# Optimization experiments

Measured on AMD Instinct MI355X. Metric: run time of the kernel, lower is better.

The kernel has to match this reference:

```python
import jax, jax.numpy as jnp
import numpy as np
from jax.scipy.special import gammaln, xlogy

B, L, C = 8, 1024, 1536
H, KD, VD = 8, 64, 192
NF = 192              # num_features for relative positional basis
FS = NF // 6          # feat_size per basis family (each family emits 2*FS cols)
SCALE = KD ** -0.5


def _pos_basis(seq_len):
    """Enformer-style basis: [exp, central_mask, gamma], each concat'd with sign copy.
    Returns [2*seq_len-1, NF] float32 constants (no learnable params)."""
    positions = jnp.arange(-(seq_len - 1), seq_len, dtype=jnp.float32)
    seq_length = float(seq_len)
    ap = jnp.abs(positions)[:, None]                      # [2L-1, 1]
    # exponential decay features
    half_life = 2.0 ** jnp.linspace(3.0, np.log2(seq_length), FS)
    f_exp = jnp.exp(-jnp.log(2.0) / half_life * ap)       # [2L-1, FS]
    # central mask features
    cw = 2.0 ** jnp.arange(1, FS + 1, dtype=jnp.float32) - 1.0
    f_cm = (cw > ap).astype(jnp.float32)
    # gamma pdf features
    stddev = seq_length / (2.0 * FS)
    start_mean = seq_length / FS
    mean = jnp.linspace(start_mean, seq_length, FS)
    conc = (mean / stddev) ** 2
    rate = mean / stddev ** 2
    log_pdf = xlogy(conc - 1.0, ap) - rate * ap - gammaln(conc) + conc * jnp.log(rate)
    pdf = jnp.exp(log_pdf) + 1e-8
    f_g = pdf / jnp.max(pdf)
    sign = jnp.sign(positions)[:, None]
    feats = [f_exp, f_cm, f_g]
    return jnp.concatenate([jnp.concatenate([f, sign * f], axis=-1) for f in feats], axis=-1)


def _rel_shift(x):
    # x: [b, h, s, f]; Transformer-XL relative shift via pad+reshape.
    b, h, s, f = x.shape
    x = jnp.pad(x, ((0, 0), (0, 0), (0, 0), (1, 0)))
    x = x.reshape(b, h, f + 1, s)
    return x[:, :, 1:s + 1, :]


def setup_inputs() -> dict:
    key = jax.random.key(0)
    ks = jax.random.split(key, 12)
    s_in = C ** -0.5
    s_hv = (H * VD) ** -0.5
    s_nf = NF ** -0.5
    return {
        "x":  jax.random.normal(ks[0], (B, L, C), jnp.float32),
        "Wq": jax.random.normal(ks[1], (C, H * KD), jnp.float32) * s_in,
        "bq": jnp.zeros((H * KD,), jnp.float32),
        "Wk": jax.random.normal(ks[2], (C, H * KD), jnp.float32) * s_in,
        "bk": jnp.zeros((H * KD,), jnp.float32),
        "Wv": jax.random.normal(ks[3], (C, H * VD), jnp.float32) * s_in,
        "bv": jnp.zeros((H * VD,), jnp.float32),
        "Wo": jax.random.normal(ks[4], (H * VD, C), jnp.float32) * s_hv,
        "bo": jnp.zeros((C,), jnp.float32),
        "WR": jax.random.normal(ks[5], (NF, KD), jnp.float32) * s_nf,
        "u":  jax.random.normal(ks[6], (H, KD), jnp.float32) * 0.02,
        "v":  jax.random.normal(ks[7], (H, KD), jnp.float32) * 0.02,
    }


def reference(x, Wq, bq, Wk, bk, Wv, bv, Wo, bo, WR, u, v):
    b, s, c = x.shape
    Q = (x @ Wq + bq).reshape(b, s, H, KD).transpose(0, 2, 1, 3)   # [b,h,s,kd]
    K = (x @ Wk + bk).reshape(b, s, H, KD).transpose(0, 2, 1, 3)
    V = (x @ Wv + bv).reshape(b, s, H, VD).transpose(0, 2, 1, 3)
    R = _pos_basis(s) @ WR                                          # [2s-1, kd]
    term1 = jnp.einsum('bhqd,bhkd->bhqk', Q, K)                     # content-content
    term2 = _rel_shift(jnp.einsum('bhqd,rd->bhqr', Q, R))           # content-position
    term3 = jnp.einsum('hd,bhkd->bhk', u, K)[:, :, None, :]         # global content bias
    term4 = _rel_shift(jnp.einsum('hd,rd->hr', v, R)[None, :, None, :])  # [1,h,1,1]
    attn = jax.nn.softmax((term1 + term2 + term3 + term4) * SCALE, axis=-1)
    out = jnp.einsum('bhqk,bhkv->bhqv', attn, V)
    out = out.transpose(0, 2, 1, 3).reshape(b, s, H * VD)
    return out @ Wo + bo
```

## Files before the change

### kernel.cpp

```cpp
#include <hip/hip_runtime.h>
#include <cstdint>
#include <cstddef>

typedef float f32x4 __attribute__((ext_vector_type(4)));
typedef short bf16x8 __attribute__((ext_vector_type(8)));

#define DEVI __device__ __forceinline__

namespace {

constexpr int BB = 8, LL = 1024, CC = 1536;
constexpr int HH = 8, KDIM = 64, VDIM = 192;
constexpr int NFEAT = 192, FSZ = 32;
constexpr float SCL = 0.125f;
constexpr int MR = BB * LL;
constexpr int NQK = HH * KDIM;
constexpr int NVD = HH * VDIM;
constexpr int NQKV = 2 * NQK + NVD;

DEVI short f2bf(float f) {
  unsigned u = __float_as_uint(f);
  u = (u + 0x7FFFu + ((u >> 16) & 1u)) >> 16;
  return (short)u;
}

DEVI void gload_lds16(const void* g, void* l) {
  __builtin_amdgcn_global_load_lds(
      (const __attribute__((address_space(1))) void*)g,
      (__attribute__((address_space(3))) void*)l, 16, 0, 0);
}

__global__ void k_f32_to_bf16(const float* __restrict__ src, short* __restrict__ dst, int n) {
  int i0 = (blockIdx.x * blockDim.x + threadIdx.x) * 4;
  int stride = gridDim.x * blockDim.x * 4;
  for (int i = i0; i < n; i += stride) {
    float4 v = *reinterpret_cast<const float4*>(src + i);
    short4 o = { f2bf(v.x), f2bf(v.y), f2bf(v.z), f2bf(v.w) };
    *reinterpret_cast<short4*>(dst + i) = o;
  }
}

__global__ void k_transpose_all(const float* __restrict__ s0, short* __restrict__ d0,
                                const float* __restrict__ s1, short* __restrict__ d1,
                                const float* __restrict__ s2, short* __restrict__ d2,
                                const float* __restrict__ s3, short* __restrict__ d3) {
  __shared__ float tile[32][33];
  int idx = blockIdx.x;
  const float* src; short* dst; int R, Cd, gx, local;
  if (idx < 768)       { src = s0; dst = d0; R = CC;  Cd = NQK; gx = 16; local = idx; }
  else if (idx < 1536) { src = s1; dst = d1; R = CC;  Cd = NQK; gx = 16; local = idx - 768; }
  else if (idx < 3840) { src = s2; dst = d2; R = CC;  Cd = NVD; gx = 48; local = idx - 1536; }
  else                 { src = s3; dst = d3; R = NVD; Cd = CC;  gx = 48; local = idx - 3840; }
  int c0 = (local % gx) * 32, r0 = (local / gx) * 32;
  int tx = threadIdx.x, ty = threadIdx.y;
  #pragma unroll
  for (int i = 0; i < 4; i++)
    tile[ty + i * 8][tx] = src[(size_t)(r0 + ty + i * 8) * Cd + c0 + tx];
  __syncthreads();
  #pragma unroll
  for (int i = 0; i < 4; i++)
    dst[(size_t)(c0 + ty + i * 8) * R + r0 + tx] = f2bf(tile[tx][ty + i * 8]);
}

__global__ void k_pdfmax(unsigned* slot) {
  int tid = blockIdx.x * blockDim.x + threadIdx.x;
  int nth = gridDim.x * blockDim.x;
  double lmax = 0.0;
  for (int idx = tid; idx < 2047 * FSZ; idx += nth) {
    int j = idx >> 5, i = idx & 31;
    double ap = (double)(j >= 1023 ? j - 1023 : 1023 - j);
    double mean = 32.0 + 32.0 * (double)i;
    double conc = (mean * (1.0 / 16.0)) * (mean * (1.0 / 16.0));
    double rate = mean * (1.0 / 256.0);
    double lp = (conc - 1.0) * log(ap) - rate * ap - lgamma(conc) + conc * log(rate);
    double pdf = exp(lp) + 1e-8;
    lmax = fmax(lmax, pdf);
  }
  float fv = (float)lmax;
  #pragma unroll
  for (int o = 32; o > 0; o >>= 1) fv = fmaxf(fv, __shfl_down(fv, o, 64));
  if ((threadIdx.x & 63) == 0) atomicMax(slot, __float_as_uint(fv));
}

__global__ void k_build_r(const float* __restrict__ WR, const unsigned* __restrict__ slot,
                          short* __restrict__ rbuf) {
  __shared__ float feats[NFEAT];
  int jp = blockIdx.x;
  int tid = threadIdx.x;
  if (jp == 0) {
    if (tid < KDIM) rbuf[tid] = 0;
    return;
  }
  int j = jp - 1;
  int pos = j - (LL - 1);
  int api = pos < 0 ? -pos : pos;
  double ap = (double)api;
  float sgn = pos > 0 ? 1.0f : (pos < 0 ? -1.0f : 0.0f);
  if (tid < FSZ) {
    double xhl = 3.0 + 7.0 * (double)tid / 31.0;
    double hl = exp2(xhl);
    float fe = (float)exp2(-ap / hl);
    feats[tid] = fe; feats[FSZ + tid] = sgn * fe;
  } else if (tid < 2 * FSZ) {
    int i = tid - FSZ;
    double cw = exp2((double)(i + 1)) - 1.0;
    float fc = cw > ap ? 1.0f : 0.0f;
    feats[2 * FSZ + i] = fc; feats[3 * FSZ + i] = sgn * fc;
  } else if (tid < 3 * FSZ) {
    int i = tid - 2 * FSZ;
    double mean = 32.0 + 32.0 * (double)i;
    double conc = (mean * (1.0 / 16.0)) * (mean * (1.0 / 16.0));
    double rate = mean * (1.0 / 256.0);
    double lp = (conc - 1.0) * log(ap) - rate * ap - lgamma(conc) + conc * log(rate);
    double pdf = exp(lp) + 1e-8;
    float fg = (float)(pdf / (double)__uint_as_float(*slot));
    feats[4 * FSZ + i] = fg; feats[5 * FSZ + i] = sgn * fg;
  }
  __syncthreads();
  if (tid < KDIM) {
    float acc = 0.f;
    #pragma unroll 4
    for (int f = 0; f < NFEAT; f++) acc += feats[f] * WR[f * KDIM + tid];
    rbuf[jp * KDIM + tid] = f2bf(acc);
  }
}

template<int MODE>
__global__ __launch_bounds__(256, 2)
void k_gemm2(const short* __restrict__ A, const short* __restrict__ Bt,
             int Ndim, int Kdim,
             const float* __restrict__ c0, const float* __restrict__ c1,
             const float* __restrict__ c2, const float* __restrict__ c3,
             void* __restrict__ D0, void* __restrict__ D1,
             void* __restrict__ D2, void* __restrict__ D3) {
  __shared__ short sA[2][128][64];
  __shared__ short sB[2][128][64];

  int bid = blockIdx.x;
  int xcd = bid & 7;
  int s = bid >> 3;
  int mt = xcd * 8 + (s & 7);
  int nt = s >> 3;
  int m0 = mt * 128, n0 = nt * 128;
  int tid = threadIdx.x;
  int w = tid >> 6, l = tid & 63;
  int hi = l >> 4, lc = l & 15;
  int wr = (w >> 1) * 64, wc = (w & 1) * 64;

  int srow = l >> 3;
  int schunk = ((l & 7) ^ srow) * 8;
  const short* gA = A + (size_t)(m0 + srow) * Kdim + schunk;
  const short* gB = Bt + (size_t)(n0 + srow) * Kdim + schunk;

  f32x4 acc[4][4] = {};
  int T = Kdim >> 6;

  auto stage = [&](int d, int k0) {
    #pragma unroll
    for (int j = 0; j < 4; j++) {
      int rb = (j * 4 + w) * 8;
      gload_lds16(gA + (size_t)rb * Kdim + k0, &sA[d][rb][0]);
      gload_lds16(gB + (size_t)rb * Kdim + k0, &sB[d][rb][0]);
    }
  };

  stage(0, 0);
  __syncthreads();

  int swz8 = (lc & 7) << 3;
  for (int t = 0; t < T; ++t) {
    int buf = t & 1;
    if (t + 1 < T) stage(buf ^ 1, (t + 1) << 6);

    #pragma unroll
    for (int kk = 0; kk < 2; kk++) {
      bf16x8 af[4], bfr[4];
      #pragma unroll
      for (int ni = 0; ni < 4; ni++)
        bfr[ni] = *(const bf16x8*)&sB[buf][wc + ni * 16 + lc][(kk * 32 + hi * 8) ^ swz8];
      #pragma unroll
      for (int mi = 0; mi < 4; mi++)
        af[mi] = *(const bf16x8*)&sA[buf][wr + mi * 16 + lc][(kk * 32 + hi * 8) ^ swz8];
      __builtin_amdgcn_s_setprio(1);
      #pragma unroll
      for (int mi = 0; mi < 4; mi++)
        #pragma unroll
        for (int ni = 0; ni < 4; ni++)
          acc[mi][ni] = __builtin_amdgcn_mfma_f32_16x16x32_bf16(af[mi], bfr[ni], acc[mi][ni], 0, 0, 0);
      __builtin_amdgcn_s_setprio(0);
    }
    __syncthreads();
  }

  #pragma unroll
  for (int ni = 0; ni < 4; ni++) {
    int col = n0 + wc + ni * 16 + lc;
    if (MODE == 0) {
      if (col < NQK) {
        float bb = c0[col], uv = c3[col];
        #pragma unroll
        for (int mi = 0; mi < 4; mi++)
          #pragma unroll
          for (int rr = 0; rr < 4; rr++) {
            int row = m0 + wr + mi * 16 + hi * 4 + rr;
            float v = acc[mi][ni][rr] + bb;
            ((short*)D0)[(size_t)row * NQK + col] = f2bf(v * SCL);
            ((short*)D1)[(size_t)row * NQK + col] = f2bf((v + uv) * SCL);
          }
      } else if (col < 2 * NQK) {
        int c = col - NQK;
        float bb = c1[c];
        #pragma unroll
        for (int mi = 0; mi < 4; mi++)
          #pragma unroll
          for (int rr = 0; rr < 4; rr++) {
            int row = m0 + wr + mi * 16 + hi * 4 + rr;
            ((short*)D2)[(size_t)row * NQK + c] = f2bf(acc[mi][ni][rr] + bb);
          }
      } else {
        int c = col - 2 * NQK;
        int hh = c / VDIM, vv = c - hh * VDIM;
        float bb = c2[c];
        int bI = m0 >> 10;
        short* vt = (short*)D3 + ((size_t)(bI * 8 + hh) * VDIM + vv) * LL;
        int sbase = (m0 & (LL - 1)) + wr + hi * 4;
        #pragma unroll
        for (int mi = 0; mi < 4; mi++) {
          short4 o = { f2bf(acc[mi][ni][0] + bb), f2bf(acc[mi][ni][1] + bb),
                       f2bf(acc[mi][ni][2] + bb), f2bf(acc[mi][ni][3] + bb) };
          *(short4*)&vt[sbase + mi * 16] = o;
        }
      }
    } else {
      float bb = c0[col];
      #pragma unroll
      for (int mi = 0; mi < 4; mi++)
        #pragma unroll
        for (int rr = 0; rr < 4; rr++) {
          int row = m0 + wr + mi * 16 + hi * 4 + rr;
          ((float*)D0)[(size_t)row * Ndim + col] = acc[mi][ni][rr] + bb;
        }
    }
  }
}

__global__ __launch_bounds__(256, 2)
void k_attn(const short* __restrict__ Qp, const short* __restrict__ Qs,
            const short* __restrict__ Kb, const short* __restrict__ Vt,
            const short* __restrict__ Rb, short* __restrict__ AO) {
  __shared__ short sK[2][64][64];
  __shared__ short sV[2][192][64];
  __shared__ short sP[128][64];

  int bid = blockIdx.x;
  int swz = (bid & 7) * 64 + (bid >> 3);
  int qt = swz & 7, bh = swz >> 3;
  int b = bh >> 3, h = bh & 7;
  int q0 = qt * 128;
  int tid = threadIdx.x;
  int w = tid >> 6, l = tid & 63;
  int hi = l >> 4, lc = l & 15;

  int base = (w & 1) * 64;
  int par = w >> 1;
  int rbase = par ? 0 : 1024;

  bf16x8 aq1[2][2], aq2[2][2];
  #pragma unroll
  for (int mi = 0; mi < 2; mi++) {
    int qglob = q0 + base + par + 2 * (mi * 16 + lc);
    const short* qpg = Qp + (size_t)(b * LL + qglob) * NQK + h * KDIM;
    aq1[mi][0] = *(const bf16x8*)&qpg[hi * 8];
    aq1[mi][1] = *(const bf16x8*)&qpg[32 + hi * 8];
    int qsrow = q0 / 2 + base / 2 + par + mi * 16 + lc;
    const short* qsg = Qs + (size_t)(b * LL + qsrow) * NQK + h * KDIM;
    aq2[mi][0] = *(const bf16x8*)&qsg[hi * 8];
    aq2[mi][1] = *(const bf16x8*)&qsg[32 + hi * 8];
  }

  const short* kg = Kb + (size_t)(b * LL) * NQK + h * KDIM;
  const short* vg = Vt + (size_t)bh * VDIM * LL;
  const short* rg = Rb + (size_t)rbase * KDIM;

  int srow = l >> 3;
  int schunk = ((l & 7) ^ srow) * 8;

  float mrun[2][4], lrun[2][4];
  #pragma unroll
  for (int mi = 0; mi < 2; mi++)
    #pragma unroll
    for (int r = 0; r < 4; r++) { mrun[mi][r] = -INFINITY; lrun[mi][r] = 0.f; }
  f32x4 oacc[2][12] = {};

  #pragma unroll
  for (int j = 0; j < 2; j++) {
    int rb2 = (j * 4 + w) * 8;
    gload_lds16(kg + (size_t)(rb2 + srow) * NQK + schunk, &sK[0][rb2][0]);
  }
  #pragma unroll
  for (int j = 0; j < 6; j++) {
    int rb2 = (j * 4 + w) * 8;
    gload_lds16(vg + (size_t)(rb2 + srow) * LL + schunk, &sV[0][rb2][0]);
  }
  __syncthreads();

  int swzk = (lc & 7) << 3;

  for (int t = 0; t < 16; t++) {
    int k0 = t * 64;
    int bf = t & 1;

    if (t < 15) {
      int kn = k0 + 64;
      #pragma unroll
      for (int j = 0; j < 2; j++) {
        int rb2 = (j * 4 + w) * 8;
        gload_lds16(kg + (size_t)(kn + rb2 + srow) * NQK + schunk, &sK[bf ^ 1][rb2][0]);
      }
      #pragma unroll
      for (int j = 0; j < 6; j++) {
        int rb2 = (j * 4 + w) * 8;
        gload_lds16(vg + (size_t)(rb2 + srow) * LL + kn + schunk, &sV[bf ^ 1][rb2][0]);
      }
    }

    bf16x8 br[2][4];
    #pragma unroll
    for (int kk = 0; kk < 2; kk++)
      #pragma unroll
      for (int ni = 0; ni < 4; ni++)
        br[kk][ni] = *(const bf16x8*)&rg[(size_t)(k0 + ni * 16 + lc) * KDIM + kk * 32 + hi * 8];

    f32x4 s[2][4] = {};
    #pragma unroll
    for (int kk = 0; kk < 2; kk++) {
      #pragma unroll
      for (int ni = 0; ni < 4; ni++) {
        bf16x8 bk = *(const bf16x8*)&sK[bf][ni * 16 + lc][(kk * 32 + hi * 8) ^ swzk];
        #pragma unroll
        for (int mi = 0; mi < 2; mi++) {
          s[mi][ni] = __builtin_amdgcn_mfma_f32_16x16x32_bf16(aq1[mi][kk], bk, s[mi][ni], 0, 0, 0);
          s[mi][ni] = __builtin_amdgcn_mfma_f32_16x16x32_bf16(aq2[mi][kk], br[kk][ni], s[mi][ni], 0, 0, 0);
        }
      }
    }

    float lmx[2][4];
    float dmax = -INFINITY;
    #pragma unroll
    for (int mi = 0; mi < 2; mi++) {
      #pragma unroll
      for (int r = 0; r < 4; r++) {
        float m3 = fmaxf(fmaxf(s[mi][0][r], s[mi][1][r]), fmaxf(s[mi][2][r], s[mi][3][r]));
        lmx[mi][r] = m3;
        dmax = fmaxf(dmax, m3 - mrun[mi][r]);
      }
    }

    if (__any(dmax > 8.0f)) {
      #pragma unroll
      for (int mi = 0; mi < 2; mi++) {
        #pragma unroll
        for (int r = 0; r < 4; r++) {
          float m3 = lmx[mi][r];
          m3 = fmaxf(m3, __shfl_xor(m3, 1, 64));
          m3 = fmaxf(m3, __shfl_xor(m3, 2, 64));
          m3 = fmaxf(m3, __shfl_xor(m3, 4, 64));
          m3 = fmaxf(m3, __shfl_xor(m3, 8, 64));
          float mnew = fmaxf(mrun[mi][r], m3);
          float fc = __expf(mrun[mi][r] - mnew);
          mrun[mi][r] = mnew;
          lrun[mi][r] *= fc;
          #pragma unroll
          for (int ni = 0; ni < 12; ni++)
            oacc[mi][ni][r] *= fc;
        }
      }
    }

    #pragma unroll
    for (int mi = 0; mi < 2; mi++) {
      #pragma unroll
      for (int r = 0; r < 4; r++) {
        int prow = w * 32 + mi * 16 + 4 * hi + r;
        int pxor = ((4 * hi + r) & 7) << 3;
        float ps = 0.f;
        #pragma unroll
        for (int ni = 0; ni < 4; ni++) {
          float p = __expf(s[mi][ni][r] - mrun[mi][r]);
          ps += p;
          sP[prow][(ni * 16 + lc) ^ pxor] = f2bf(p);
        }
        lrun[mi][r] += ps;
      }
    }

    __builtin_amdgcn_s_setprio(1);
    #pragma unroll
    for (int kk = 0; kk < 2; kk++) {
      bf16x8 pa[2];
      #pragma unroll
      for (int mi = 0; mi < 2; mi++)
        pa[mi] = *(const bf16x8*)&sP[w * 32 + mi * 16 + lc][(kk * 32 + hi * 8) ^ swzk];
      #pragma unroll
      for (int ni = 0; ni < 12; ni++) {
        bf16x8 bv = *(const bf16x8*)&sV[bf][ni * 16 + lc][(kk * 32 + hi * 8) ^ swzk];
        #pragma unroll
        for (int mi = 0; mi < 2; mi++)
          oacc[mi][ni] = __builtin_amdgcn_mfma_f32_16x16x32_bf16(pa[mi], bv, oacc[mi][ni], 0, 0, 0);
      }
    }
    __builtin_amdgcn_s_setprio(0);

    __syncthreads();
  }

  #pragma unroll
  for (int mi = 0; mi < 2; mi++) {
    #pragma unroll
    for (int r = 0; r < 4; r++) {
      float L = lrun[mi][r];
      L += __shfl_xor(L, 1, 64);
      L += __shfl_xor(L, 2, 64);
      L += __shfl_xor(L, 4, 64);
      L += __shfl_xor(L, 8, 64);
      float iv = 1.0f / L;
      int qglob = q0 + base + par + 2 * (mi * 16 + 4 * hi + r);
      short* ao = AO + (size_t)(b * LL + qglob) * NVD + h * VDIM;
      #pragma unroll
      for (int ni = 0; ni < 12; ni++)
        ao[ni * 16 + lc] = f2bf(oacc[mi][ni][r] * iv);
    }
  }
}

}

extern "C" void kernel_launch(void* const* d_in, const int* in_sizes, int n_in,
                              void* d_out, int out_size, void* d_ws, size_t ws_size,
                              hipStream_t stream) {
  (void)in_sizes; (void)n_in; (void)out_size; (void)ws_size;
  const float* x  = (const float*)d_in[0];
  const float* Wq = (const float*)d_in[1];
  const float* bq = (const float*)d_in[2];
  const float* Wk = (const float*)d_in[3];
  const float* bk = (const float*)d_in[4];
  const float* Wv = (const float*)d_in[5];
  const float* bv = (const float*)d_in[6];
  const float* Wo = (const float*)d_in[7];
  const float* bo = (const float*)d_in[8];
  const float* WR = (const float*)d_in[9];
  const float* uu = (const float*)d_in[10];

  char* ws = (char*)d_ws;
  size_t off = 0;
  auto alloc = [&](size_t bytes) -> void* {
    void* p = ws + off;
    off += (bytes + 255) & ~(size_t)255;
    return p;
  };
  short* RB      = (short*)alloc((size_t)2048 * 64 * 2);
  unsigned* PMAX = (unsigned*)alloc(256);
  short* XB      = (short*)alloc((size_t)MR * CC * 2);
  short* WALL    = (short*)alloc((size_t)NQKV * CC * 2);
  short* WOT     = (short*)alloc((size_t)CC * NVD * 2);
  short* QP      = (short*)alloc((size_t)MR * NQK * 2);
  short* QS      = (short*)alloc((size_t)MR * NQK * 2);
  short* KB      = (short*)alloc((size_t)MR * NQK * 2);
  short* VT      = (short*)alloc((size_t)MR * NVD * 2);
  short* AO      = (short*)alloc((size_t)MR * NVD * 2);

  short* WQT = WALL;
  short* WKT = WALL + (size_t)NQK * CC;
  short* WVT = WALL + (size_t)(2 * NQK) * CC;

  hipMemsetAsync(PMAX, 0, 4, stream);
  k_f32_to_bf16<<<2048, 256, 0, stream>>>(x, XB, MR * CC);
  k_transpose_all<<<6144, dim3(32, 8), 0, stream>>>(Wq, WQT, Wk, WKT, Wv, WVT, Wo, WOT);
  k_pdfmax<<<64, 256, 0, stream>>>(PMAX);
  k_build_r<<<2048, 256, 0, stream>>>(WR, PMAX, RB);
  k_gemm2<0><<<dim3(MR / 128 * (NQKV / 128)), 256, 0, stream>>>(
      XB, WALL, NQKV, CC, bq, bk, bv, uu, QS, QP, KB, VT);
  k_attn<<<dim3(LL / 128 * BB * HH), 256, 0, stream>>>(QP, QS, KB, VT, RB, AO);
  k_gemm2<1><<<dim3(MR / 128 * (CC / 128)), 256, 0, stream>>>(
      AO, WOT, CC, NVD, bo, nullptr, nullptr, nullptr, d_out, nullptr, nullptr, nullptr);
}
```

Before: 265.3 us.

## Triple-buffer GEMM K-loop with BK=32 and compute gamma pdf max on host

The projection GEMMs switch from a double-buffered BK=64 K-loop to a triple-buffered BK=32 pipeline with two stages in flight. They use explicit vmcnt waits plus raw barriers in place of __syncthreads, a new LDS swizzle, and launch bounds raised to three blocks per CU. The aim is to hide global-to-LDS latency better and raise occupancy. Separately, the gamma-pdf normaliser, a pure constant, is computed on the host by checking points near each distribution's mode, which removes the k_pdfmax kernel and the memset. The host max assumes the mode-neighbourhood search finds the true maximum, and the halved K tile doubles the number of barriers per GEMM.

```diff
diff --git a/kernel.cpp b/kernel.cpp
--- a/kernel.cpp
+++ b/kernel.cpp
@@ -1,6 +1,7 @@
 #include <hip/hip_runtime.h>
 #include <cstdint>
 #include <cstddef>
+#include <cmath>
 
 typedef float f32x4 __attribute__((ext_vector_type(4)));
 typedef short bf16x8 __attribute__((ext_vector_type(8)));
@@ -62,27 +63,7 @@
     dst[(size_t)(c0 + ty + i * 8) * R + r0 + tx] = f2bf(tile[tx][ty + i * 8]);
 }
 
-__global__ void k_pdfmax(unsigned* slot) {
-  int tid = blockIdx.x * blockDim.x + threadIdx.x;
-  int nth = gridDim.x * blockDim.x;
-  double lmax = 0.0;
-  for (int idx = tid; idx < 2047 * FSZ; idx += nth) {
-    int j = idx >> 5, i = idx & 31;
-    double ap = (double)(j >= 1023 ? j - 1023 : 1023 - j);
-    double mean = 32.0 + 32.0 * (double)i;
-    double conc = (mean * (1.0 / 16.0)) * (mean * (1.0 / 16.0));
-    double rate = mean * (1.0 / 256.0);
-    double lp = (conc - 1.0) * log(ap) - rate * ap - lgamma(conc) + conc * log(rate);
-    double pdf = exp(lp) + 1e-8;
-    lmax = fmax(lmax, pdf);
-  }
-  float fv = (float)lmax;
-  #pragma unroll
-  for (int o = 32; o > 0; o >>= 1) fv = fmaxf(fv, __shfl_down(fv, o, 64));
-  if ((threadIdx.x & 63) == 0) atomicMax(slot, __float_as_uint(fv));
-}
-
-__global__ void k_build_r(const float* __restrict__ WR, const unsigned* __restrict__ slot,
+__global__ void k_build_r(const float* __restrict__ WR, float pmax,
                           short* __restrict__ rbuf) {
   __shared__ float feats[NFEAT];
   int jp = blockIdx.x;
@@ -113,7 +94,7 @@
     double rate = mean * (1.0 / 256.0);
     double lp = (conc - 1.0) * log(ap) - rate * ap - lgamma(conc) + conc * log(rate);
     double pdf = exp(lp) + 1e-8;
-    float fg = (float)(pdf / (double)__uint_as_float(*slot));
+    float fg = (float)(pdf / (double)pmax);
     feats[4 * FSZ + i] = fg; feats[5 * FSZ + i] = sgn * fg;
   }
   __syncthreads();
@@ -126,15 +107,15 @@
 }
 
 template<int MODE>
-__global__ __launch_bounds__(256, 2)
-void k_gemm2(const short* __restrict__ A, const short* __restrict__ Bt,
+__global__ __launch_bounds__(256, 3)
+void k_gemm3(const short* __restrict__ A, const short* __restrict__ Bt,
              int Ndim, int Kdim,
              const float* __restrict__ c0, const float* __restrict__ c1,
              const float* __restrict__ c2, const float* __restrict__ c3,
              void* __restrict__ D0, void* __restrict__ D1,
              void* __restrict__ D2, void* __restrict__ D3) {
-  __shared__ short sA[2][128][64];
-  __shared__ short sB[2][128][64];
+  __shared__ short sA[3][128][32];
+  __shared__ short sB[3][128][32];
 
   int bid = blockIdx.x;
   int xcd = bid & 7;
@@ -147,49 +128,54 @@
   int hi = l >> 4, lc = l & 15;
   int wr = (w >> 1) * 64, wc = (w & 1) * 64;
 
-  int srow = l >> 3;
-  int schunk = ((l & 7) ^ srow) * 8;
-  const short* gA = A + (size_t)(m0 + srow) * Kdim + schunk;
-  const short* gB = Bt + (size_t)(n0 + srow) * Kdim + schunk;
+  int rowoff = l >> 2;
+  int schunk = ((l & 3) ^ ((l >> 3) & 3)) * 8;
+  const short* gA = A + (size_t)(m0 + rowoff) * Kdim + schunk;
+  const short* gB = Bt + (size_t)(n0 + rowoff) * Kdim + schunk;
 
   f32x4 acc[4][4] = {};
-  int T = Kdim >> 6;
-
-  auto stage = [&](int d, int k0) {
-    #pragma unroll
-    for (int j = 0; j < 4; j++) {
-      int rb = (j * 4 + w) * 8;
-      gload_lds16(gA + (size_t)rb * Kdim + k0, &sA[d][rb][0]);
-      gload_lds16(gB + (size_t)rb * Kdim + k0, &sB[d][rb][0]);
+  int T = Kdim >> 5;
+
+  auto stage = [&](int d, int kt) {
+    #pragma unroll
+    for (int j = 0; j < 2; j++) {
+      int rb = j * 64 + w * 16;
+      gload_lds16(gA + (size_t)rb * Kdim + kt * 32, &sA[d][rb][0]);
+      gload_lds16(gB + (size_t)rb * Kdim + kt * 32, &sB[d][rb][0]);
     }
   };
 
   stage(0, 0);
-  __syncthreads();
-
-  int swz8 = (lc & 7) << 3;
+  stage(1, 1);
+  asm volatile("s_waitcnt vmcnt(4)" ::: "memory");
+  __builtin_amdgcn_s_barrier();
+  __builtin_amdgcn_sched_barrier(0);
+
+  int rswz = (lc >> 1) & 3;
   for (int t = 0; t < T; ++t) {
-    int buf = t & 1;
-    if (t + 1 < T) stage(buf ^ 1, (t + 1) << 6);
-
-    #pragma unroll
-    for (int kk = 0; kk < 2; kk++) {
-      bf16x8 af[4], bfr[4];
+    int buf = t % 3;
+    bool more = (t + 2) < T;
+    if (more) stage((t + 2) % 3, t + 2);
+
+    bf16x8 af[4], bfr[4];
+    #pragma unroll
+    for (int ni = 0; ni < 4; ni++)
+      bfr[ni] = *(const bf16x8*)&sB[buf][wc + ni * 16 + lc][(hi ^ rswz) * 8];
+    #pragma unroll
+    for (int mi = 0; mi < 4; mi++)
+      af[mi] = *(const bf16x8*)&sA[buf][wr + mi * 16 + lc][(hi ^ rswz) * 8];
+    __builtin_amdgcn_s_setprio(1);
+    #pragma unroll
+    for (int mi = 0; mi < 4; mi++)
       #pragma unroll
       for (int ni = 0; ni < 4; ni++)
-        bfr[ni] = *(const bf16x8*)&sB[buf][wc + ni * 16 + lc][(kk * 32 + hi * 8) ^ swz8];
-      #pragma unroll
-      for (int mi = 0; mi < 4; mi++)
-        af[mi] = *(const bf16x8*)&sA[buf][wr + mi * 16 + lc][(kk * 32 + hi * 8) ^ swz8];
-      __builtin_amdgcn_s_setprio(1);
-      #pragma unroll
-      for (int mi = 0; mi < 4; mi++)
-        #pragma unroll
-        for (int ni = 0; ni < 4; ni++)
-          acc[mi][ni] = __builtin_amdgcn_mfma_f32_16x16x32_bf16(af[mi], bfr[ni], acc[mi][ni], 0, 0, 0);
-      __builtin_amdgcn_s_setprio(0);
-    }
-    __syncthreads();
+        acc[mi][ni] = __builtin_amdgcn_mfma_f32_16x16x32_bf16(af[mi], bfr[ni], acc[mi][ni], 0, 0, 0);
+    __builtin_amdgcn_s_setprio(0);
+
+    if (more) asm volatile("s_waitcnt vmcnt(4)" ::: "memory");
+    else      asm volatile("s_waitcnt vmcnt(0)" ::: "memory");
+    __builtin_amdgcn_s_barrier();
+    __builtin_amdgcn_sched_barrier(0);
   }
 
   #pragma unroll
@@ -452,6 +438,25 @@
   const float* WR = (const float*)d_in[9];
   const float* uu = (const float*)d_in[10];
 
+  double pmaxd = 0.0;
+  for (int i = 0; i < 32; i++) {
+    double mean = 32.0 + 32.0 * (double)i;
+    double conc = (mean / 16.0) * (mean / 16.0);
+    double rate = mean / 256.0;
+    double mode = (conc - 1.0) / rate;
+    long m0i = (long)floor(mode);
+    for (long dj = -2; dj <= 2; dj++) {
+      long ap = m0i + dj;
+      if (ap < 1) ap = 1;
+      if (ap > 1023) ap = 1023;
+      double lp = (conc - 1.0) * log((double)ap) - rate * (double)ap
+                  - lgamma(conc) + conc * log(rate);
+      double pdf = exp(lp) + 1e-8;
+      if (pdf > pmaxd) pmaxd = pdf;
+    }
+  }
+  float pmax = (float)pmaxd;
+
   char* ws = (char*)d_ws;
   size_t off = 0;
   auto alloc = [&](size_t bytes) -> void* {
@@ -460,7 +465,6 @@
     return p;
   };
   short* RB      = (short*)alloc((size_t)2048 * 64 * 2);
-  unsigned* PMAX = (unsigned*)alloc(256);
   short* XB      = (short*)alloc((size_t)MR * CC * 2);
   short* WALL    = (short*)alloc((size_t)NQKV * CC * 2);
   short* WOT     = (short*)alloc((size_t)CC * NVD * 2);
@@ -474,14 +478,12 @@
   short* WKT = WALL + (size_t)NQK * CC;
   short* WVT = WALL + (size_t)(2 * NQK) * CC;
 
-  hipMemsetAsync(PMAX, 0, 4, stream);
   k_f32_to_bf16<<<2048, 256, 0, stream>>>(x, XB, MR * CC);
   k_transpose_all<<<6144, dim3(32, 8), 0, stream>>>(Wq, WQT, Wk, WKT, Wv, WVT, Wo, WOT);
-  k_pdfmax<<<64, 256, 0, stream>>>(PMAX);
-  k_build_r<<<2048, 256, 0, stream>>>(WR, PMAX, RB);
-  k_gemm2<0><<<dim3(MR / 128 * (NQKV / 128)), 256, 0, stream>>>(
+  k_build_r<<<2048, 256, 0, stream>>>(WR, pmax, RB);
+  k_gemm3<0><<<dim3(MR / 128 * (NQKV / 128)), 256, 0, stream>>>(
       XB, WALL, NQKV, CC, bq, bk, bv, uu, QS, QP, KB, VT);
   k_attn<<<dim3(LL / 128 * BB * HH), 256, 0, stream>>>(QP, QS, KB, VT, RB, AO);
-  k_gemm2<1><<<dim3(MR / 128 * (CC / 128)), 256, 0, stream>>>(
+  k_gemm3<1><<<dim3(MR / 128 * (CC / 128)), 256, 0, stream>>>(
       AO, WOT, CC, NVD, bo, nullptr, nullptr, nullptr, d_out, nullptr, nullptr, nullptr);
 }
```

Result: faster. 244.6 us (-7.8%).
